# Kernel optimization log

Hardware: AMD Instinct MI355X
Metric: run time of the kernel (lower is better)

Reference implementation:

```python
import jax, jax.numpy as jnp
import numpy as np
from jax import lax

# Hardcoded module constants (from source)
T, B = 8, 64
CIN, C, HW, NCLS = 3, 64, 32, 10
V_INIT, V_DECAY, V_THR = 0.0, 0.8, 1.2


def conv_raw(x, w, b):
    # x: [T, B, Cin, H, W] -> conv2d per timestep, stride 1, pad 1
    t, bsz = x.shape[:2]
    xf = x.reshape((t * bsz,) + x.shape[2:])
    y = lax.conv_general_dilated(
        xf, w, window_strides=(1, 1), padding=[(1, 1), (1, 1)],
        dimension_numbers=('NCHW', 'OIHW', 'NCHW'))
    y = y + b[None, :, None, None]
    return y.reshape((t, bsz) + y.shape[1:])


def lif(i_cur):
    # NOTE: original code reads v[t] from the v_init-initialized tensor each
    # step (not v[t-1]), so there is NO temporal recurrence: v = v_init*decay + I[t]
    v = V_INIT * V_DECAY + i_cur
    return (v >= V_THR).astype(i_cur.dtype)


def setup_inputs() -> dict:
    key = jax.random.key(0)
    ks = jax.random.split(key, 7)
    spike_input = jax.random.uniform(ks[0], (T, B, CIN, HW, HW), jnp.float32)
    # original uses plain torch.randn for weights and biases
    w1 = jax.random.normal(ks[1], (C, CIN, 3, 3), jnp.float32)
    b1 = jax.random.normal(ks[2], (C,), jnp.float32)
    w2 = jax.random.normal(ks[3], (C, C, 3, 3), jnp.float32)
    b2 = jax.random.normal(ks[4], (C,), jnp.float32)
    wfc = jax.random.normal(ks[5], (NCLS, C * HW * HW), jnp.float32)
    bfc = jax.random.normal(ks[6], (NCLS,), jnp.float32)
    return {"spike_input": spike_input, "w1": w1, "b1": b1,
            "w2": w2, "b2": b2, "wfc": wfc, "bfc": bfc}


def reference(spike_input, w1, b1, w2, b2, wfc, bfc):
    x = lif(conv_raw(spike_input, w1, b1))      # [T,B,64,32,32] binary spikes
    x = lif(conv_raw(x, w2, b2))                # [T,B,64,32,32]
    x = x.reshape(T, B, -1)                     # [T,B,64*32*32]
    out = jnp.einsum('tbi,oi->tbo', x, wfc) + bfc
    return out.sum(0)                           # [B, 10]
```

## Files before the change

kernel.cpp:

```cpp
#include <hip/hip_runtime.h>
#include <hip/hip_bf16.h>


typedef __attribute__((ext_vector_type(8))) short bf16x8;
typedef __attribute__((ext_vector_type(4))) float f32x4;
typedef __attribute__((ext_vector_type(4))) int   i32x4;

#define S1Q (5.5f/127.0f)
#define S2Q (S1Q/254.0f)

static const size_t SZ_IMG  = 65536;
static const size_t OFF_S8  = 0;
static const size_t OFF_CNT = 512*SZ_IMG;
static const size_t OFF_W1F = OFF_CNT + (4u<<20);
static const size_t OFF_BQ  = OFF_W1F + 8192;

#define SWZ(cp) (((cp) >> 1) & 3)

__device__ __forceinline__ void gl_lds16(const void* g, void* l) {
  __builtin_amdgcn_global_load_lds(
      (const __attribute__((address_space(1))) unsigned int*)g,
      (__attribute__((address_space(3))) unsigned int*)l, 16, 0, 0);
}

__global__ __launch_bounds__(256) void kprep(
    const float* __restrict__ w1, const float* __restrict__ w2,
    short* __restrict__ W1F, signed char* __restrict__ Bq)
{
  int i = blockIdx.x*256 + threadIdx.x;
  if (i < 4096) {
    int t2 = i >> 11, r = i & 2047, co = r >> 5, k = r & 31;
    short out = 0;
    if (k < 27) {
      int s = k/3, ci = k - s*3;
      float w = w1[co*27 + ci*9 + s];
      __hip_bfloat16 h = __float2bfloat16(w);
      if (t2 == 0) out = *(short*)&h;
      else { __hip_bfloat16 lo = __float2bfloat16(w - (float)h); out = *(short*)&lo; }
    }
    W1F[i] = out;
  }
  if (i < 36864) {
    int co = i/576, rem = i - co*576, ci = rem/9, s = rem - ci*9;
    float w = w2[i];
    int q1 = (int)roundf(w * (1.0f/S1Q)); q1 = q1 > 127 ? 127 : (q1 < -127 ? -127 : q1);
    float r1 = w - S1Q*(float)q1;
    int q2 = (int)roundf(r1 * (1.0f/S2Q)); q2 = q2 > 127 ? 127 : (q2 < -127 ? -127 : q2);
    int off = s*4096 + co*64 + ci;
    Bq[off] = (signed char)q1; Bq[36864 + off] = (signed char)q2;
  }
}

__global__ __launch_bounds__(256, 2) void conv1_k(
    const float* __restrict__ x, const short* __restrict__ W1F,
    const float* __restrict__ b1, unsigned char* __restrict__ S8)
{
  const int img = blockIdx.x;
  const int tid = threadIdx.x;
  const int w   = tid >> 6;
  const int l   = tid & 63;
  const int lm  = l & 15, lk = l >> 4;

  __shared__ int xt4[7344];
  __shared__ i32x4 bnc4[4][16][4];
  unsigned short* xs = (unsigned short*)xt4;
  unsigned char*  bnc = (unsigned char*)bnc4;

  for (int i = tid; i < 7344; i += 256) xt4[i] = 0;
  __syncthreads();
  const float* xin = x + (size_t)img * 3072;
  for (int j = tid; j < 3072; j += 256) {
    int ci = j >> 10, r = (j >> 5) & 31, c = j & 31;
    float f = xin[j];
    __hip_bfloat16 h = __float2bfloat16(f);
    __hip_bfloat16 lo = __float2bfloat16(f - (float)h);
    int idx = ci*1224 + (r+1)*36 + (c+1);
    xs[idx] = *(unsigned short*)&h;
    xs[idx + 7344] = *(unsigned short*)&lo;
  }
  __syncthreads();

  bf16x8 Wf[2][4];
  float  b1v[4];
  #pragma unroll
  for (int t2 = 0; t2 < 2; t2++)
    #pragma unroll
    for (int nf = 0; nf < 4; nf++)
      Wf[t2][nf] = *(const bf16x8*)(W1F + t2*2048 + (nf*16+lm)*32 + lk*8);
  #pragma unroll
  for (int nf = 0; nf < 4; nf++) b1v[nf] = b1[nf*16 + lm];

  int off16[8];
  #pragma unroll
  for (int e = 0; e < 8; e++) {
    int k = lk*8 + e;
    if (k < 27) { int s = k/3, ci = k - s*3, dr = s/3, dc = s - dr*3;
                  off16[e] = ci*1224 + dr*36 + dc; }
    else off16[e] = 0;
  }

  unsigned char* S8b = S8 + (size_t)img * SZ_IMG;
  for (int fi = 0; fi < 16; fi++) {
    const int pxF = w*16 + fi;
    const int row = pxF >> 1, colh = pxF & 1;
    const int base16 = row*36 + colh*16 + lm;
    bf16x8 ah, al;
    #pragma unroll
    for (int e = 0; e < 8; e++) {
      int idx = base16 + off16[e];
      ah[e] = (short)xs[idx];
      al[e] = (short)xs[idx + 7344];
    }
    f32x4 acc[4] = {};
    #pragma unroll
    for (int nf = 0; nf < 4; nf++) {
      acc[nf] = __builtin_amdgcn_mfma_f32_16x16x32_bf16(ah, Wf[0][nf], acc[nf], 0,0,0);
      acc[nf] = __builtin_amdgcn_mfma_f32_16x16x32_bf16(al, Wf[0][nf], acc[nf], 0,0,0);
      acc[nf] = __builtin_amdgcn_mfma_f32_16x16x32_bf16(ah, Wf[1][nf], acc[nf], 0,0,0);
      acc[nf] = __builtin_amdgcn_mfma_f32_16x16x32_bf16(al, Wf[1][nf], acc[nf], 0,0,0);
    }
    #pragma unroll
    for (int nf = 0; nf < 4; nf++)
      #pragma unroll
      for (int e4 = 0; e4 < 4; e4++) {
        float v = acc[nf][e4] + b1v[nf];
        bnc[w*1024 + (lk*4+e4)*64 + nf*16 + lm] = (v >= 1.2f) ? 1 : 0;
      }
    const int pxl = l >> 2, coq = l & 3;
    i32x4 sp = *(const i32x4*)(bnc + w*1024 + pxl*64 + coq*16);
    const int gcol = colh*16 + pxl;
    const int cq = coq ^ SWZ(gcol + 1);
    *(i32x4*)(S8b + (size_t)(row*32 + gcol)*64 + cq*16) = sp;
  }
}

__global__ __launch_bounds__(512, 2) void conv2_k(
    const unsigned char* __restrict__ S8, const signed char* __restrict__ Bq,
    const float* __restrict__ b2, unsigned char* __restrict__ cnt)
{
  __shared__ __align__(16) unsigned char Abuf[2][21760];
  const int j  = blockIdx.x;
  const int b  = ((j >> 3) & 7) * 8 + (j & 7);
  const int rq = j >> 6;
  const int tid = threadIdx.x;
  const int wv = tid >> 6, l = tid & 63;
  const int lm = l & 15, lk = l >> 4;
  const int ch = wv >> 2;
  const int wr = wv & 3;

  i32x4 Bf[2][9][2];
  #pragma unroll
  for (int q = 0; q < 2; q++)
    #pragma unroll
    for (int s = 0; s < 9; s++)
      #pragma unroll
      for (int nf = 0; nf < 2; nf++)
        Bf[q][s][nf] = *(const i32x4*)(Bq + q*36864 + s*4096 + (ch*32+nf*16+lm)*64 + lk*16);
  const float b2v[2] = { b2[ch*32 + lm], b2[ch*32 + 16 + lm] };

  {
    i32x4 z = {0,0,0,0};
    i32x4* ap = (i32x4*)Abuf;
    #pragma unroll
    for (int it = 0; it < 6; it++) { int c = it*512 + tid; if (c < 2720) ap[c] = z; }
  }
  __syncthreads();

  {
    const unsigned char* Simg = S8 + (size_t)(0*64 + b)*SZ_IMG;
    if (wv < 5) {
      #pragma unroll
      for (int rr = 0; rr < 2; rr++) {
        const int lr = wv*2 + rr;
        const int grow = rq*8 - 1 + lr;
        if (grow >= 0 && grow < 32) {
          const unsigned char* src = Simg + grow*2048 + l*16;
          unsigned char* dst = &Abuf[0][lr*2176 + 64];
          gl_lds16(src, dst);
          gl_lds16(src + 1024, dst + 1024);
        }
      }
    }
  }
  __syncthreads();

  unsigned int cntp[4][2] = {};

  for (int t = 0; t < 8; t++) {
    if (t < 7 && wv < 5) {
      const unsigned char* Simg = S8 + (size_t)((t+1)*64 + b)*SZ_IMG;
      unsigned char* bufn = Abuf[(t+1) & 1];
      #pragma unroll
      for (int rr = 0; rr < 2; rr++) {
        const int lr = wv*2 + rr;
        const int grow = rq*8 - 1 + lr;
        if (grow >= 0 && grow < 32) {
          const unsigned char* src = Simg + grow*2048 + l*16;
          unsigned char* dst = bufn + lr*2176 + 64;
          gl_lds16(src, dst);
          gl_lds16(src + 1024, dst + 1024);
        }
      }
    }

    const unsigned char* ab = Abuf[t & 1];
    i32x4 acc1[4][2] = {}, acc2[4][2] = {};
    #pragma unroll
    for (int s = 0; s < 9; s++) {
      const int dr = s/3, dc = s - dr*3;
      #pragma unroll
      for (int a = 0; a < 4; a++) {
        const int lr = 2*wr + (a>>1) + dr;
        const int cp = ((a&1)<<4) + lm + dc;
        i32x4 Af = *(const i32x4*)(ab + lr*2176 + cp*64 + ((lk ^ SWZ(cp)) << 4));
        #pragma unroll
        for (int nf = 0; nf < 2; nf++) {
          acc1[a][nf] = __builtin_amdgcn_mfma_i32_16x16x64_i8(Af, Bf[0][s][nf], acc1[a][nf],0,0,0);
          acc2[a][nf] = __builtin_amdgcn_mfma_i32_16x16x64_i8(Af, Bf[1][s][nf], acc2[a][nf],0,0,0);
        }
      }
    }

    #pragma unroll
    for (int a = 0; a < 4; a++)
      #pragma unroll
      for (int nf = 0; nf < 2; nf++) {
        unsigned int p = 0;
        #pragma unroll
        for (int e = 0; e < 4; e++) {
          float v = S1Q*(float)acc1[a][nf][e] + S2Q*(float)acc2[a][nf][e] + b2v[nf];
          p |= (v >= 1.2f ? 1u : 0u) << (8*e);
        }
        cntp[a][nf] += p;
      }
    __syncthreads();
  }

  unsigned char* bb = (unsigned char*)Abuf;
  #pragma unroll
  for (int a = 0; a < 4; a++) {
    const int orow = 2*wr + (a>>1);
    const int colb = ((a&1)<<4) + lk*4;
    #pragma unroll
    for (int nf = 0; nf < 2; nf++) {
      const int co = ch*32 + nf*16 + lm;
      *(unsigned int*)(bb + co*256 + orow*32 + colb) = cntp[a][nf];
    }
  }
  __syncthreads();
  #pragma unroll
  for (int it = 0; it < 2; it++) {
    const int c = it*512 + tid;
    const int co = c >> 4, inner = (c & 15) << 4;
    *(i32x4*)(cnt + (size_t)(b*64 + co)*1024 + rq*256 + inner) =
        *(const i32x4*)(bb + co*256 + inner);
  }
}

__global__ __launch_bounds__(256) void fc_k(
    const unsigned char* __restrict__ cnt, const float* __restrict__ wfc,
    const float* __restrict__ bfc, float* __restrict__ out)
{
  const int b = blockIdx.x & 63;
  const int chunk = blockIdx.x >> 6;
  const int tid = threadIdx.x;
  float acc[10];
  #pragma unroll
  for (int o = 0; o < 10; o++) acc[o] = 0.f;
  const int i4base = chunk*4096 + tid;
  for (int w = 0; w < 16; w++) {
    int i4 = i4base + w*256;
    uchar4 cv = *(const uchar4*)(cnt + (size_t)b*65536 + i4*4);
    float c0 = cv.x, c1 = cv.y, c2 = cv.z, c3 = cv.w;
    #pragma unroll
    for (int o = 0; o < 10; o++) {
      float4 wv = *(const float4*)(wfc + (size_t)o*65536 + i4*4);
      acc[o] += wv.x*c0 + wv.y*c1 + wv.z*c2 + wv.w*c3;
    }
  }
  __shared__ float red[10][256];
  #pragma unroll
  for (int o = 0; o < 10; o++) red[o][tid] = acc[o];
  __syncthreads();
  for (int off = 128; off > 0; off >>= 1) {
    if (tid < off) {
      #pragma unroll
      for (int o = 0; o < 10; o++) red[o][tid] += red[o][tid + off];
    }
    __syncthreads();
  }
  if (tid < 10) {
    float v = red[tid][0];
    if (chunk == 0) v += 8.0f * bfc[tid];
    atomicAdd(out + b*10 + tid, v);
  }
}

extern "C" void kernel_launch(void* const* d_in, const int* in_sizes, int n_in,
                              void* d_out, int out_size, void* d_ws, size_t ws_size,
                              hipStream_t stream)
{
  const float* x   = (const float*)d_in[0];
  const float* w1  = (const float*)d_in[1];
  const float* b1  = (const float*)d_in[2];
  const float* w2  = (const float*)d_in[3];
  const float* b2  = (const float*)d_in[4];
  const float* wfc = (const float*)d_in[5];
  const float* bfc = (const float*)d_in[6];
  float* out = (float*)d_out;

  unsigned char* ws  = (unsigned char*)d_ws;
  unsigned char* S8  = ws + OFF_S8;
  unsigned char* cnt = ws + OFF_CNT;
  short*         W1F = (short*)(ws + OFF_W1F);
  signed char*   Bq  = (signed char*)(ws + OFF_BQ);

  hipMemsetAsync(out, 0, 64*10*sizeof(float), stream);
  kprep<<<144, 256, 0, stream>>>(w1, w2, W1F, Bq);
  conv1_k<<<512, 256, 0, stream>>>(x, W1F, b1, S8);
  conv2_k<<<256, 512, 0, stream>>>(S8, Bq, b2, cnt);
  fc_k<<<256, 256, 0, stream>>>(cnt, wfc, bfc, out);
}
```

Measured before the change: 143.7 us.

## Split conv work into finer blocks and restructure FC reduction for occupancy

conv1 now splits each image into two row halves, so twice as many blocks each stage a smaller padded input in LDS. conv2 now covers 4 output rows per block with each wave owning 16 output channels, which halves its register and LDS footprint, and it raises MFMA priority during the inner loop. The count tile is stored through an XOR-swizzled LDS layout. The FC kernel now has each wave handle two batch images and reuse the loaded weights, and it replaces the shared-memory tree reduction with wave shuffles and atomics. The goal is more occupancy and parallelism on a 256-CU part, at the cost of extra halo loads, duplicated weight fragment loads, and more atomics.

```diff
diff --git a/kernel.cpp b/kernel.cpp
--- a/kernel.cpp
+++ b/kernel.cpp
@@ -51,32 +51,34 @@
   }
 }
 
-__global__ __launch_bounds__(256, 2) void conv1_k(
+__global__ __launch_bounds__(256, 4) void conv1_k(
     const float* __restrict__ x, const short* __restrict__ W1F,
     const float* __restrict__ b1, unsigned char* __restrict__ S8)
 {
-  const int img = blockIdx.x;
+  const int j   = blockIdx.x;
+  const int img = j & 511, rh = j >> 9;
   const int tid = threadIdx.x;
   const int w   = tid >> 6;
   const int l   = tid & 63;
   const int lm  = l & 15, lk = l >> 4;
 
-  __shared__ int xt4[7344];
+  __shared__ int xt4[1944];
   __shared__ i32x4 bnc4[4][16][4];
   unsigned short* xs = (unsigned short*)xt4;
   unsigned char*  bnc = (unsigned char*)bnc4;
 
-  for (int i = tid; i < 7344; i += 256) xt4[i] = 0;
+  for (int i = tid; i < 1944; i += 256) xt4[i] = 0;
   __syncthreads();
   const float* xin = x + (size_t)img * 3072;
-  for (int j = tid; j < 3072; j += 256) {
-    int ci = j >> 10, r = (j >> 5) & 31, c = j & 31;
-    float f = xin[j];
+  for (int jj = tid; jj < 1728; jj += 256) {
+    int ci = jj / 576, rem = jj - ci*576, rl = rem >> 5, c = rem & 31;
+    int gr = rh*16 - 1 + rl;
+    float f = (gr >= 0 && gr < 32) ? xin[ci*1024 + gr*32 + c] : 0.f;
     __hip_bfloat16 h = __float2bfloat16(f);
     __hip_bfloat16 lo = __float2bfloat16(f - (float)h);
-    int idx = ci*1224 + (r+1)*36 + (c+1);
+    int idx = ci*648 + rl*36 + (c+1);
     xs[idx] = *(unsigned short*)&h;
-    xs[idx + 7344] = *(unsigned short*)&lo;
+    xs[idx + 1944] = *(unsigned short*)&lo;
   }
   __syncthreads();
 
@@ -95,21 +97,21 @@
   for (int e = 0; e < 8; e++) {
     int k = lk*8 + e;
     if (k < 27) { int s = k/3, ci = k - s*3, dr = s/3, dc = s - dr*3;
-                  off16[e] = ci*1224 + dr*36 + dc; }
+                  off16[e] = ci*648 + dr*36 + dc; }
     else off16[e] = 0;
   }
 
   unsigned char* S8b = S8 + (size_t)img * SZ_IMG;
-  for (int fi = 0; fi < 16; fi++) {
-    const int pxF = w*16 + fi;
-    const int row = pxF >> 1, colh = pxF & 1;
-    const int base16 = row*36 + colh*16 + lm;
+  for (int fi = 0; fi < 8; fi++) {
+    const int pxF = w*8 + fi;
+    const int lrow = pxF >> 1, colh = pxF & 1;
+    const int base16 = lrow*36 + colh*16 + lm;
     bf16x8 ah, al;
     #pragma unroll
     for (int e = 0; e < 8; e++) {
       int idx = base16 + off16[e];
       ah[e] = (short)xs[idx];
-      al[e] = (short)xs[idx + 7344];
+      al[e] = (short)xs[idx + 1944];
     }
     f32x4 acc[4] = {};
     #pragma unroll
@@ -129,131 +131,108 @@
     const int pxl = l >> 2, coq = l & 3;
     i32x4 sp = *(const i32x4*)(bnc + w*1024 + pxl*64 + coq*16);
     const int gcol = colh*16 + pxl;
+    const int grow = rh*16 + lrow;
     const int cq = coq ^ SWZ(gcol + 1);
-    *(i32x4*)(S8b + (size_t)(row*32 + gcol)*64 + cq*16) = sp;
-  }
-}
-
-__global__ __launch_bounds__(512, 2) void conv2_k(
+    *(i32x4*)(S8b + (size_t)(grow*32 + gcol)*64 + cq*16) = sp;
+  }
+}
+
+__global__ __launch_bounds__(512, 4) void conv2_k(
     const unsigned char* __restrict__ S8, const signed char* __restrict__ Bq,
     const float* __restrict__ b2, unsigned char* __restrict__ cnt)
 {
-  __shared__ __align__(16) unsigned char Abuf[2][21760];
+  __shared__ __align__(16) unsigned char Abuf[2][13056];
   const int j  = blockIdx.x;
-  const int b  = ((j >> 3) & 7) * 8 + (j & 7);
-  const int rq = j >> 6;
+  const int b  = j & 63;
+  const int rs = j >> 6;
   const int tid = threadIdx.x;
   const int wv = tid >> 6, l = tid & 63;
   const int lm = l & 15, lk = l >> 4;
-  const int ch = wv >> 2;
-  const int wr = wv & 3;
-
-  i32x4 Bf[2][9][2];
+  const int cq = wv & 3;
+  const int rp = wv >> 2;
+
+  i32x4 Bf[2][9];
   #pragma unroll
   for (int q = 0; q < 2; q++)
     #pragma unroll
     for (int s = 0; s < 9; s++)
-      #pragma unroll
-      for (int nf = 0; nf < 2; nf++)
-        Bf[q][s][nf] = *(const i32x4*)(Bq + q*36864 + s*4096 + (ch*32+nf*16+lm)*64 + lk*16);
-  const float b2v[2] = { b2[ch*32 + lm], b2[ch*32 + 16 + lm] };
+      Bf[q][s] = *(const i32x4*)(Bq + q*36864 + s*4096 + (cq*16+lm)*64 + lk*16);
+  const float b2v = b2[cq*16 + lm];
 
   {
     i32x4 z = {0,0,0,0};
     i32x4* ap = (i32x4*)Abuf;
-    #pragma unroll
-    for (int it = 0; it < 6; it++) { int c = it*512 + tid; if (c < 2720) ap[c] = z; }
-  }
-  __syncthreads();
-
-  {
-    const unsigned char* Simg = S8 + (size_t)(0*64 + b)*SZ_IMG;
-    if (wv < 5) {
-      #pragma unroll
-      for (int rr = 0; rr < 2; rr++) {
-        const int lr = wv*2 + rr;
-        const int grow = rq*8 - 1 + lr;
-        if (grow >= 0 && grow < 32) {
-          const unsigned char* src = Simg + grow*2048 + l*16;
-          unsigned char* dst = &Abuf[0][lr*2176 + 64];
-          gl_lds16(src, dst);
-          gl_lds16(src + 1024, dst + 1024);
-        }
-      }
-    }
-  }
-  __syncthreads();
-
-  unsigned int cntp[4][2] = {};
+    for (int c = tid; c < 1632; c += 512) ap[c] = z;
+  }
+  __syncthreads();
+
+  if (wv < 6) {
+    const int grow = rs*4 - 1 + wv;
+    if (grow >= 0 && grow < 32) {
+      const unsigned char* src = S8 + (size_t)b*SZ_IMG + grow*2048 + l*16;
+      unsigned char* dst = &Abuf[0][wv*2176 + 64];
+      gl_lds16(src, dst);
+      gl_lds16(src + 1024, dst + 1024);
+    }
+  }
+  __syncthreads();
+
+  unsigned int cntp[4] = {};
 
   for (int t = 0; t < 8; t++) {
-    if (t < 7 && wv < 5) {
-      const unsigned char* Simg = S8 + (size_t)((t+1)*64 + b)*SZ_IMG;
-      unsigned char* bufn = Abuf[(t+1) & 1];
-      #pragma unroll
-      for (int rr = 0; rr < 2; rr++) {
-        const int lr = wv*2 + rr;
-        const int grow = rq*8 - 1 + lr;
-        if (grow >= 0 && grow < 32) {
-          const unsigned char* src = Simg + grow*2048 + l*16;
-          unsigned char* dst = bufn + lr*2176 + 64;
-          gl_lds16(src, dst);
-          gl_lds16(src + 1024, dst + 1024);
-        }
+    if (t < 7 && wv < 6) {
+      const int grow = rs*4 - 1 + wv;
+      if (grow >= 0 && grow < 32) {
+        const unsigned char* src = S8 + (size_t)((t+1)*64 + b)*SZ_IMG + grow*2048 + l*16;
+        unsigned char* dst = &Abuf[(t+1) & 1][wv*2176 + 64];
+        gl_lds16(src, dst);
+        gl_lds16(src + 1024, dst + 1024);
       }
     }
 
     const unsigned char* ab = Abuf[t & 1];
-    i32x4 acc1[4][2] = {}, acc2[4][2] = {};
+    i32x4 acc1[4] = {}, acc2[4] = {};
+    __builtin_amdgcn_s_setprio(1);
     #pragma unroll
     for (int s = 0; s < 9; s++) {
       const int dr = s/3, dc = s - dr*3;
       #pragma unroll
       for (int a = 0; a < 4; a++) {
-        const int lr = 2*wr + (a>>1) + dr;
+        const int lr = rp*2 + (a>>1) + dr;
         const int cp = ((a&1)<<4) + lm + dc;
         i32x4 Af = *(const i32x4*)(ab + lr*2176 + cp*64 + ((lk ^ SWZ(cp)) << 4));
-        #pragma unroll
-        for (int nf = 0; nf < 2; nf++) {
-          acc1[a][nf] = __builtin_amdgcn_mfma_i32_16x16x64_i8(Af, Bf[0][s][nf], acc1[a][nf],0,0,0);
-          acc2[a][nf] = __builtin_amdgcn_mfma_i32_16x16x64_i8(Af, Bf[1][s][nf], acc2[a][nf],0,0,0);
-        }
-      }
-    }
-
-    #pragma unroll
-    for (int a = 0; a < 4; a++)
-      #pragma unroll
-      for (int nf = 0; nf < 2; nf++) {
-        unsigned int p = 0;
-        #pragma unroll
-        for (int e = 0; e < 4; e++) {
-          float v = S1Q*(float)acc1[a][nf][e] + S2Q*(float)acc2[a][nf][e] + b2v[nf];
-          p |= (v >= 1.2f ? 1u : 0u) << (8*e);
-        }
-        cntp[a][nf] += p;
-      }
+        acc1[a] = __builtin_amdgcn_mfma_i32_16x16x64_i8(Af, Bf[0][s], acc1[a], 0,0,0);
+        acc2[a] = __builtin_amdgcn_mfma_i32_16x16x64_i8(Af, Bf[1][s], acc2[a], 0,0,0);
+      }
+    }
+    __builtin_amdgcn_s_setprio(0);
+
+    #pragma unroll
+    for (int a = 0; a < 4; a++) {
+      unsigned int p = 0;
+      #pragma unroll
+      for (int e = 0; e < 4; e++) {
+        float v = S1Q*(float)acc1[a][e] + S2Q*(float)acc2[a][e] + b2v;
+        p |= (v >= 1.2f ? 1u : 0u) << (8*e);
+      }
+      cntp[a] += p;
+    }
     __syncthreads();
   }
 
-  unsigned char* bb = (unsigned char*)Abuf;
+  unsigned int* bb = (unsigned int*)Abuf;
   #pragma unroll
   for (int a = 0; a < 4; a++) {
-    const int orow = 2*wr + (a>>1);
-    const int colb = ((a&1)<<4) + lk*4;
-    #pragma unroll
-    for (int nf = 0; nf < 2; nf++) {
-      const int co = ch*32 + nf*16 + lm;
-      *(unsigned int*)(bb + co*256 + orow*32 + colb) = cntp[a][nf];
-    }
-  }
-  __syncthreads();
-  #pragma unroll
-  for (int it = 0; it < 2; it++) {
-    const int c = it*512 + tid;
-    const int co = c >> 4, inner = (c & 15) << 4;
-    *(i32x4*)(cnt + (size_t)(b*64 + co)*1024 + rq*256 + inner) =
-        *(const i32x4*)(bb + co*256 + inner);
+    const int lrow = rp*2 + (a>>1);
+    const int u = lrow*8 + (a&1)*4 + lk;
+    const int co = cq*16 + lm;
+    bb[co*32 + (((u>>2) ^ (co&7))<<2) + (u&3)] = cntp[a];
+  }
+  __syncthreads();
+  {
+    const int co = tid >> 3, tc = tid & 7;
+    i32x4 v = *(const i32x4*)(bb + co*32 + ((tc ^ (co&7)) << 2));
+    *(i32x4*)(cnt + (size_t)(b*64 + co)*1024 + rs*128 + tc*16) = v;
   }
 }
 
@@ -261,38 +240,46 @@
     const unsigned char* __restrict__ cnt, const float* __restrict__ wfc,
     const float* __restrict__ bfc, float* __restrict__ out)
 {
-  const int b = blockIdx.x & 63;
-  const int chunk = blockIdx.x >> 6;
+  const int ig = blockIdx.x & 63;
+  const int bg = blockIdx.x >> 6;
   const int tid = threadIdx.x;
-  float acc[10];
-  #pragma unroll
-  for (int o = 0; o < 10; o++) acc[o] = 0.f;
-  const int i4base = chunk*4096 + tid;
-  for (int w = 0; w < 16; w++) {
-    int i4 = i4base + w*256;
-    uchar4 cv = *(const uchar4*)(cnt + (size_t)b*65536 + i4*4);
-    float c0 = cv.x, c1 = cv.y, c2 = cv.z, c3 = cv.w;
+  const int w = tid >> 6, l = tid & 63;
+  const int b0 = bg*8 + w*2;
+
+  float acc[2][10] = {};
+  #pragma unroll
+  for (int k = 0; k < 4; k++) {
+    const int i4 = ig*256 + k*64 + l;
+    float4 wv[10];
+    #pragma unroll
+    for (int o = 0; o < 10; o++)
+      wv[o] = *(const float4*)(wfc + (size_t)o*65536 + (size_t)i4*4);
+    #pragma unroll
+    for (int bb = 0; bb < 2; bb++) {
+      uchar4 cv = *(const uchar4*)(cnt + (size_t)(b0+bb)*65536 + (size_t)i4*4);
+      float c0 = cv.x, c1 = cv.y, c2 = cv.z, c3 = cv.w;
+      #pragma unroll
+      for (int o = 0; o < 10; o++)
+        acc[bb][o] += wv[o].x*c0 + wv[o].y*c1 + wv[o].z*c2 + wv[o].w*c3;
+    }
+  }
+  #pragma unroll
+  for (int bb = 0; bb < 2; bb++)
     #pragma unroll
     for (int o = 0; o < 10; o++) {
-      float4 wv = *(const float4*)(wfc + (size_t)o*65536 + i4*4);
-      acc[o] += wv.x*c0 + wv.y*c1 + wv.z*c2 + wv.w*c3;
-    }
-  }
-  __shared__ float red[10][256];
-  #pragma unroll
-  for (int o = 0; o < 10; o++) red[o][tid] = acc[o];
-  __syncthreads();
-  for (int off = 128; off > 0; off >>= 1) {
-    if (tid < off) {
-      #pragma unroll
-      for (int o = 0; o < 10; o++) red[o][tid] += red[o][tid + off];
-    }
-    __syncthreads();
-  }
-  if (tid < 10) {
-    float v = red[tid][0];
-    if (chunk == 0) v += 8.0f * bfc[tid];
-    atomicAdd(out + b*10 + tid, v);
+      float v = acc[bb][o];
+      for (int off = 32; off > 0; off >>= 1) v += __shfl_down(v, off, 64);
+      acc[bb][o] = v;
+    }
+  if (l == 0) {
+    #pragma unroll
+    for (int bb = 0; bb < 2; bb++)
+      #pragma unroll
+      for (int o = 0; o < 10; o++) {
+        float v = acc[bb][o];
+        if (ig == 0) v += 8.0f * bfc[o];
+        atomicAdd(out + (b0+bb)*10 + o, v);
+      }
   }
 }
 
@@ -317,7 +304,7 @@
 
   hipMemsetAsync(out, 0, 64*10*sizeof(float), stream);
   kprep<<<144, 256, 0, stream>>>(w1, w2, W1F, Bq);
-  conv1_k<<<512, 256, 0, stream>>>(x, W1F, b1, S8);
-  conv2_k<<<256, 512, 0, stream>>>(S8, Bq, b2, cnt);
-  fc_k<<<256, 256, 0, stream>>>(cnt, wfc, bfc, out);
-}
+  conv1_k<<<1024, 256, 0, stream>>>(x, W1F, b1, S8);
+  conv2_k<<<512, 512, 0, stream>>>(S8, Bq, b2, cnt);
+  fc_k<<<512, 256, 0, stream>>>(cnt, wfc, bfc, out);
+}
```

After: 176.7 us. 1.23x slower.
